# Optimization experiments

Measured on AMD Instinct MI355X. Metric: run time of the kernel, lower is better.

Reference implementation:

```python
import jax, jax.numpy as jnp
import numpy as np

N = 50000      # nodes
E = 600000     # edges
D = 128        # num_features == hidden_units
L = 4          # num_layers
C = 10         # num_classes
G = 512        # graphs in batch
BN_EPS = 1e-5


def setup_inputs() -> dict:
    key = jax.random.key(0)
    ks = jax.random.split(key, 10)
    x = jax.random.normal(ks[0], (N, D), dtype=jnp.float32)
    src = jax.random.randint(ks[1], (E,), 0, N)
    dst = jax.random.randint(ks[2], (E,), 0, N)
    edge_index = jnp.stack([src, dst]).astype(jnp.int64)
    batch = jnp.sort(jax.random.randint(ks[3], (N,), 0, G)).astype(jnp.int64)
    s = 1.0 / np.sqrt(D)
    Wc1 = jax.random.uniform(ks[4], (L, D, D), jnp.float32, -s, s)
    bc1 = jnp.zeros((L, D), jnp.float32)
    Wc2 = jax.random.uniform(ks[5], (L, D, D), jnp.float32, -s, s)
    bc2 = jnp.zeros((L, D), jnp.float32)
    g_mid = jnp.ones((L, D), jnp.float32)   # BN gamma inside conv MLP
    b_mid = jnp.zeros((L, D), jnp.float32)
    g_out = jnp.ones((L, D), jnp.float32)   # BN gamma after conv
    b_out = jnp.zeros((L, D), jnp.float32)
    fcW = jax.random.uniform(ks[6], (L + 1, D, C), jnp.float32, -s, s)
    fcb = jnp.zeros((L + 1, C), jnp.float32)
    return dict(x=x, edge_index=edge_index, batch=batch, Wc1=Wc1, bc1=bc1,
                Wc2=Wc2, bc2=bc2, g_mid=g_mid, b_mid=b_mid, g_out=g_out,
                b_out=b_out, fcW=fcW, fcb=fcb)


def _bn(h, gamma, beta):
    # training-mode BatchNorm1d over the node axis (biased variance)
    mu = h.mean(0)
    var = h.var(0)
    return (h - mu) * jax.lax.rsqrt(var + BN_EPS) * gamma + beta


def reference(x, edge_index, batch, Wc1, bc1, Wc2, bc2, g_mid, b_mid,
              g_out, b_out, fcW, fcb):
    src, dst = edge_index[0], edge_index[1]
    outs = [x]
    h = x
    for i in range(L):
        # GINConv (eps=0): nn( x + sum_{j in N(i)} x_j )
        agg = jax.ops.segment_sum(h[src], dst, num_segments=N)
        z = h + agg
        z = z @ Wc1[i] + bc1[i]
        z = jax.nn.relu(_bn(z, g_mid[i], b_mid[i]))
        z = z @ Wc2[i] + bc2[i]
        h = jax.nn.relu(_bn(z, g_out[i], b_out[i]))  # outer BN + ReLU
        outs.append(h)
    out = jnp.zeros((G, C), x.dtype)
    for i, o in enumerate(outs):
        pooled = jax.ops.segment_sum(o, batch, num_segments=G)  # [G, D]
        out = out + pooled @ fcW[i] + fcb[i]  # dropout p=0.0 -> identity
    return jax.nn.log_softmax(out, axis=-1)
```

## Files before the change

kernel.cpp:

```cpp
#include <hip/hip_runtime.h>
#include <hip/hip_bf16.h>

#define NN 50000
#define EE 600000
#define DD 128
#define LL 4
#define CC 10
#define GG 512
#define BN_EPS 1e-5f
#define ELLW 48

#define EB_BLOCKS ((EE + 255) / 256)
#define PW_BLOCKS ((8 * DD * DD) / 256)
#define GP_BLOCKS 3
#define AGG_BLOCKS (NN / 8)
#define ZERO_N (8 * 256 + NN)
#define ZERO_BLOCKS ((ZERO_N + 255) / 256)

typedef __attribute__((ext_vector_type(8))) short short8;
typedef __attribute__((ext_vector_type(4))) float f32x4;

__device__ __forceinline__ unsigned short f2b(float f) {
    union { float f; unsigned int u; } v; v.f = f;
    unsigned int u = v.u;
    unsigned int r = (u + 0x7fffu + ((u >> 16) & 1u)) >> 16;
    return (unsigned short)r;
}
__device__ __forceinline__ float b2f(unsigned short h) {
    union { unsigned int u; float f; } v; v.u = ((unsigned int)h) << 16;
    return v.f;
}


__global__ __launch_bounds__(256) void zero_kernel(int* __restrict__ base) {
    int i = blockIdx.x * 256 + threadIdx.x;
    if (i < ZERO_N) base[i] = 0;
}


__global__ __launch_bounds__(256) void setup_kernel(const int* __restrict__ src,
                                                    const int* __restrict__ dst,
                                                    int* __restrict__ cursor,
                                                    int* __restrict__ ell,
                                                    const float* __restrict__ Wc1,
                                                    const float* __restrict__ Wc2,
                                                    unsigned short* __restrict__ WTb,
                                                    const int* __restrict__ batch,
                                                    int* __restrict__ gptr,
                                                    const float* __restrict__ x,
                                                    unsigned short* __restrict__ xb,
                                                    float* __restrict__ pooled0) {
    int b = blockIdx.x;
    if (b < GG) {
        __shared__ float2 red[4][64];
        const int g = b;
        int lo = 0, hi = NN;
        while (lo < hi) { int mid = (lo + hi) >> 1; if (batch[mid] < g) lo = mid + 1; else hi = mid; }
        int beg = lo;
        hi = NN;
        while (lo < hi) { int mid = (lo + hi) >> 1; if (batch[mid] < g + 1) lo = mid + 1; else hi = mid; }
        int end = lo;
        int wave = threadIdx.x >> 6, lane = threadIdx.x & 63;
        float ax = 0.f, ay = 0.f;
        for (int r = beg + wave; r < end; r += 4) {
            float2 v = ((const float2*)(x + (size_t)r * DD))[lane];
            ax += v.x; ay += v.y;
            ((unsigned int*)(xb + (size_t)r * DD))[lane] =
                (unsigned int)f2b(v.x) | ((unsigned int)f2b(v.y) << 16);
        }
        red[wave][lane] = make_float2(ax, ay);
        __syncthreads();
        if (threadIdx.x < 64) {
            float2 a = red[0][lane], bb = red[1][lane], c = red[2][lane], d = red[3][lane];
            ((float2*)pooled0)[(size_t)g * 64 + lane] =
                make_float2(a.x + bb.x + c.x + d.x, a.y + bb.y + c.y + d.y);
        }
    } else if (b < GG + EB_BLOCKS) {
        int e = (b - GG) * 256 + threadIdx.x;
        if (e < EE) {
            int d = dst[e];
            int slot = atomicAdd(&cursor[d], 1);
            if (slot < ELLW) ell[(size_t)d * ELLW + slot] = src[e];
        }
    } else if (b < GG + EB_BLOCKS + PW_BLOCKS) {
        int idx = (b - GG - EB_BLOCKS) * 256 + threadIdx.x;
        int mat = idx >> 14;
        int n = (idx >> 7) & 127;
        int k = idx & 127;
        const float* srcp = (mat < 4) ? (Wc1 + (size_t)mat * DD * DD)
                                      : (Wc2 + (size_t)(mat - 4) * DD * DD);
        WTb[idx] = f2b(srcp[k * DD + n]);
    } else {
        int g = (b - GG - EB_BLOCKS - PW_BLOCKS) * 256 + threadIdx.x;
        if (g > GG) return;
        int lo = 0, hi = NN;
        while (lo < hi) {
            int mid = (lo + hi) >> 1;
            if (batch[mid] < g) lo = mid + 1; else hi = mid;
        }
        gptr[g] = lo;
    }
}


template <bool BN>
__device__ __forceinline__ void agg_pair(int nA, const unsigned short* __restrict__ hb,
                                         const int* __restrict__ ell,
                                         const int* __restrict__ degA,
                                         const float* __restrict__ stats,
                                         const float* __restrict__ gamma,
                                         const float* __restrict__ beta,
                                         unsigned short* __restrict__ outb) {
    const int lane = threadIdx.x & 63;
    const int seg = lane & 15;
    const int slot = lane >> 4;

    float A[8], B[8];
    if (BN) {
#pragma unroll
        for (int j = 0; j < 8; ++j) {
            int c = seg * 8 + j;
            float mu = stats[c] * (1.0f / NN);
            float var = stats[DD + c] * (1.0f / NN) - mu * mu;
            A[j] = gamma[c] * rsqrtf(var + BN_EPS);
            B[j] = beta[c] - mu * A[j];
        }
    }

    const uint4* hb4 = (const uint4*)hb;
    uint4 self = hb4[(size_t)(nA + (slot == 1 ? 1 : 0)) * 16 + seg];

    float accA[8], accB[8];
#pragma unroll
    for (int j = 0; j < 8; ++j) { accA[j] = 0.f; accB[j] = 0.f; }

    const int* rowA = ell + (size_t)nA * ELLW;
    const int* rowB = rowA + ELLW;
    const int dgA = min(degA[nA], ELLW);
    const int dgB = min(degA[nA + 1], ELLW);
    const int dgM = max(dgA, dgB);

    for (int e = 0; e < dgM; e += 16) {
        bool vA[4], vB[4];
        int iA[4], iB[4];
#pragma unroll
        for (int i = 0; i < 4; ++i) {
            int t = e + i * 4 + slot;
            vA[i] = (t < dgA);
            vB[i] = (t < dgB);
            iA[i] = rowA[t];
            iB[i] = rowB[t];
        }
        uint4 a[4], b[4];
#pragma unroll
        for (int i = 0; i < 4; ++i) {
            if (vA[i]) a[i] = hb4[(size_t)iA[i] * 16 + seg];
        }
#pragma unroll
        for (int i = 0; i < 4; ++i) {
            if (vB[i]) b[i] = hb4[(size_t)iB[i] * 16 + seg];
        }
#pragma unroll
        for (int i = 0; i < 4; ++i) {
            if (vA[i]) {
#pragma unroll
                for (int j = 0; j < 4; ++j) {
                    unsigned int u = ((unsigned int*)&a[i])[j];
                    float x = b2f((unsigned short)(u & 0xffff));
                    float y = b2f((unsigned short)(u >> 16));
                    if (BN) {
                        x = fmaxf(0.f, fmaf(x, A[2 * j], B[2 * j]));
                        y = fmaxf(0.f, fmaf(y, A[2 * j + 1], B[2 * j + 1]));
                    }
                    accA[2 * j] += x;
                    accA[2 * j + 1] += y;
                }
            }
            if (vB[i]) {
#pragma unroll
                for (int j = 0; j < 4; ++j) {
                    unsigned int u = ((unsigned int*)&b[i])[j];
                    float x = b2f((unsigned short)(u & 0xffff));
                    float y = b2f((unsigned short)(u >> 16));
                    if (BN) {
                        x = fmaxf(0.f, fmaf(x, A[2 * j], B[2 * j]));
                        y = fmaxf(0.f, fmaf(y, A[2 * j + 1], B[2 * j + 1]));
                    }
                    accB[2 * j] += x;
                    accB[2 * j + 1] += y;
                }
            }
        }
    }

#pragma unroll
    for (int j = 0; j < 8; ++j) {
        accA[j] += __shfl_xor(accA[j], 16);
        accA[j] += __shfl_xor(accA[j], 32);
        accB[j] += __shfl_xor(accB[j], 16);
        accB[j] += __shfl_xor(accB[j], 32);
    }

    if (slot < 2) {
        uint4 o;
#pragma unroll
        for (int j = 0; j < 4; ++j) {
            unsigned int u = ((unsigned int*)&self)[j];
            float x = b2f((unsigned short)(u & 0xffff));
            float y = b2f((unsigned short)(u >> 16));
            if (BN) {
                x = fmaxf(0.f, fmaf(x, A[2 * j], B[2 * j]));
                y = fmaxf(0.f, fmaf(y, A[2 * j + 1], B[2 * j + 1]));
            }
            float sx = (slot == 0) ? accA[2 * j] : accB[2 * j];
            float sy = (slot == 0) ? accA[2 * j + 1] : accB[2 * j + 1];
            ((unsigned int*)&o)[j] =
                (unsigned int)f2b(sx + x) | ((unsigned int)f2b(sy + y) << 16);
        }
        ((uint4*)outb)[(size_t)(nA + slot) * 16 + seg] = o;
    }
}

__global__ __launch_bounds__(256) void aggregate_x(const unsigned short* __restrict__ hb,
                                                   const int* __restrict__ ell,
                                                   const int* __restrict__ degA,
                                                   unsigned short* __restrict__ outb) {
    int nA = blockIdx.x * 8 + (threadIdx.x >> 6) * 2;
    agg_pair<false>(nA, hb, ell, degA, nullptr, nullptr, nullptr, outb);
}


__global__ __launch_bounds__(256, 2) void gemm_mfma(
    const unsigned short* __restrict__ Ab,
    const unsigned short* __restrict__ WTb,
    const float* __restrict__ bias,
    const float* __restrict__ bnStatsIn,
    const float* __restrict__ gamma, const float* __restrict__ beta,
    unsigned short* __restrict__ Outb,
    float* __restrict__ statsOut)
{
    __shared__ unsigned short As[128 * 128];
    __shared__ float AbnS[DD], BbnS[DD];
    __shared__ float colred[2][DD];

    const int tid = threadIdx.x;
    const int row0 = blockIdx.x * 128;
    const bool doBn = (bnStatsIn != nullptr);
    const int lane = tid & 63;
    const int fr = lane & 15, fq = lane >> 4;

    short8 bfrag[8][4];
#pragma unroll
    for (int n = 0; n < 8; ++n)
#pragma unroll
        for (int kk = 0; kk < 4; ++kk)
            bfrag[n][kk] = *(const short8*)((const char*)WTb + (n * 16 + fr) * 256 + kk * 64 + fq * 16);

    if (tid < DD) {
        colred[0][tid] = 0.f;
        colred[1][tid] = 0.f;
        if (doBn) {
            float mu = bnStatsIn[tid] * (1.0f / NN);
            float var = bnStatsIn[DD + tid] * (1.0f / NN) - mu * mu;
            float A = gamma[tid] * rsqrtf(var + BN_EPS);
            AbnS[tid] = A;
            BbnS[tid] = beta[tid] - mu * A;
        }
    }
    if (doBn) __syncthreads();

#pragma unroll
    for (int i = 0; i < 8; ++i) {
        int c = tid + i * 256;
        int row = c >> 4, seg = c & 15;
        int gr = row0 + row;
        uint4 v = make_uint4(0u, 0u, 0u, 0u);
        if (gr < NN) v = ((const uint4*)(Ab + (size_t)gr * DD))[seg];
        if (doBn) {
            int k0 = seg * 8;
#pragma unroll
            for (int e = 0; e < 4; ++e) {
                unsigned int u = ((unsigned int*)&v)[e];
                int cidx = k0 + 2 * e;
                float lo = fmaxf(0.f, fmaf(b2f((unsigned short)(u & 0xffff)), AbnS[cidx], BbnS[cidx]));
                float hi = fmaxf(0.f, fmaf(b2f((unsigned short)(u >> 16)), AbnS[cidx + 1], BbnS[cidx + 1]));
                ((unsigned int*)&v)[e] = (unsigned int)f2b(lo) | ((unsigned int)f2b(hi) << 16);
            }
        }
        int byte = (row * 256 + seg * 16) ^ ((row & 7) << 4);
        *(uint4*)((char*)As + byte) = v;
    }
    __syncthreads();

    const int wave = tid >> 6;
    const int wr0 = wave * 32;

    f32x4 acc[2][8];
#pragma unroll
    for (int m = 0; m < 2; ++m)
#pragma unroll
        for (int n = 0; n < 8; ++n) acc[m][n] = (f32x4)0.f;

#pragma unroll
    for (int kk = 0; kk < 4; ++kk) {
        int kbyte = kk * 64 + fq * 16;
        short8 a[2];
#pragma unroll
        for (int m = 0; m < 2; ++m) {
            int row = wr0 + m * 16 + fr;
            a[m] = *(const short8*)((const char*)As + ((row * 256 + kbyte) ^ ((row & 7) << 4)));
        }
#pragma unroll
        for (int m = 0; m < 2; ++m)
#pragma unroll
            for (int n = 0; n < 8; ++n)
                acc[m][n] = __builtin_amdgcn_mfma_f32_16x16x32_bf16(a[m], bfrag[n][kk], acc[m][n], 0, 0, 0);
    }

    float bias_n[8], s[8], q[8];
#pragma unroll
    for (int n = 0; n < 8; ++n) {
        bias_n[n] = bias[n * 16 + fr];
        s[n] = 0.f;
        q[n] = 0.f;
    }
#pragma unroll
    for (int m = 0; m < 2; ++m) {
        int rbase = row0 + wr0 + m * 16 + fq * 4;
#pragma unroll
        for (int j = 0; j < 4; ++j) {
            int gr = rbase + j;
            if (gr < NN) {
#pragma unroll
                for (int n = 0; n < 8; ++n) {
                    float o = acc[m][n][j] + bias_n[n];
                    Outb[(size_t)gr * DD + n * 16 + fr] = f2b(o);
                    s[n] += o;
                    q[n] += o * o;
                }
            }
        }
    }
#pragma unroll
    for (int n = 0; n < 8; ++n) {
        s[n] += __shfl_xor(s[n], 16);
        s[n] += __shfl_xor(s[n], 32);
        q[n] += __shfl_xor(q[n], 16);
        q[n] += __shfl_xor(q[n], 32);
    }
    if (fq == 0) {
#pragma unroll
        for (int n = 0; n < 8; ++n) {
            atomicAdd(&colred[0][n * 16 + fr], s[n]);
            atomicAdd(&colred[1][n * 16 + fr], q[n]);
        }
    }
    __syncthreads();
    if (tid < DD) {
        atomicAdd(&statsOut[tid], colred[0][tid]);
        atomicAdd(&statsOut[DD + tid], colred[1][tid]);
    }
}


template <bool LAST>
__global__ __launch_bounds__(256) void post_layer(
    const unsigned short* __restrict__ Z,
    const float* __restrict__ stats,
    const float* __restrict__ gamma,
    const float* __restrict__ beta,
    const int* __restrict__ gptr,
    const int* __restrict__ ell,
    const int* __restrict__ degA,
    float* __restrict__ pooledDst,
    unsigned short* __restrict__ aggOut,
    const float* __restrict__ pooledAll,
    const float* __restrict__ fcW,
    const float* __restrict__ fcb,
    float* __restrict__ out)
{
    const int bid = blockIdx.x;
    if (bid < GG) {
        __shared__ float2 red[4][64];
        __shared__ float p4[DD];
        const int g = bid;
        const int wave = threadIdx.x >> 6, lane = threadIdx.x & 63;
        const int c0 = lane * 2, c1 = c0 + 1;
        float mu0 = stats[c0] * (1.0f / NN);
        float var0 = stats[DD + c0] * (1.0f / NN) - mu0 * mu0;
        float A0 = gamma[c0] * rsqrtf(var0 + BN_EPS);
        float B0 = beta[c0] - mu0 * A0;
        float mu1 = stats[c1] * (1.0f / NN);
        float var1 = stats[DD + c1] * (1.0f / NN) - mu1 * mu1;
        float A1 = gamma[c1] * rsqrtf(var1 + BN_EPS);
        float B1 = beta[c1] - mu1 * A1;

        float ax = 0.f, ay = 0.f;
        int beg = gptr[g], end = gptr[g + 1];
        for (int r = beg + wave; r < end; r += 4) {
            unsigned int u = ((const unsigned int*)(Z + (size_t)r * DD))[lane];
            ax += fmaxf(0.f, fmaf(b2f((unsigned short)(u & 0xffff)), A0, B0));
            ay += fmaxf(0.f, fmaf(b2f((unsigned short)(u >> 16)), A1, B1));
        }
        red[wave][lane] = make_float2(ax, ay);
        __syncthreads();
        if (threadIdx.x < 64) {
            float2 a = red[0][lane], b = red[1][lane], c = red[2][lane], d = red[3][lane];
            float2 r2 = make_float2(a.x + b.x + c.x + d.x, a.y + b.y + c.y + d.y);
            ((float2*)pooledDst)[(size_t)g * 64 + lane] = r2;
            if (LAST) {
                p4[c0] = r2.x;
                p4[c1] = r2.y;
            }
        }
        if (LAST) {
            __syncthreads();
            if (threadIdx.x < 64) {
                float acc[CC];
#pragma unroll
                for (int c = 0; c < CC; ++c) acc[c] = 0.f;
                for (int i = 0; i < LL + 1; ++i) {
                    const float* Wf = fcW + (size_t)i * DD * CC;
                    for (int k = lane; k < DD; k += 64) {
                        float pv = (i == LL) ? p4[k] : pooledAll[((size_t)i * GG + g) * DD + k];
                        const float* wr = Wf + k * CC;
#pragma unroll
                        for (int c = 0; c < CC; ++c) acc[c] = fmaf(pv, wr[c], acc[c]);
                    }
                }
#pragma unroll
                for (int c = 0; c < CC; ++c)
                    for (int off = 32; off > 0; off >>= 1) acc[c] += __shfl_down(acc[c], off);
                if (lane == 0) {
#pragma unroll
                    for (int c = 0; c < CC; ++c) {
                        float b = 0.f;
                        for (int i = 0; i < LL + 1; ++i) b += fcb[i * CC + c];
                        acc[c] += b;
                    }
                    float m = acc[0];
#pragma unroll
                    for (int c = 1; c < CC; ++c) m = fmaxf(m, acc[c]);
                    float se = 0.f;
#pragma unroll
                    for (int c = 0; c < CC; ++c) se += expf(acc[c] - m);
                    float lse = m + logf(se);
#pragma unroll
                    for (int c = 0; c < CC; ++c) out[(size_t)g * CC + c] = acc[c] - lse;
                }
            }
        }
    } else {
        int nA = (bid - GG) * 8 + (threadIdx.x >> 6) * 2;
        agg_pair<true>(nA, Z, ell, degA, stats, gamma, beta, aggOut);
    }
}


extern "C" void kernel_launch(void* const* d_in, const int* in_sizes, int n_in,
                              void* d_out, int out_size, void* d_ws, size_t ws_size,
                              hipStream_t stream) {
    const float* x     = (const float*)d_in[0];
    const int*   ei    = (const int*)d_in[1];
    const int*   batch = (const int*)d_in[2];
    const float* Wc1   = (const float*)d_in[3];
    const float* bc1   = (const float*)d_in[4];
    const float* Wc2   = (const float*)d_in[5];
    const float* bc2   = (const float*)d_in[6];
    const float* g_mid = (const float*)d_in[7];
    const float* b_mid = (const float*)d_in[8];
    const float* g_out = (const float*)d_in[9];
    const float* b_out = (const float*)d_in[10];
    const float* fcW   = (const float*)d_in[11];
    const float* fcb   = (const float*)d_in[12];
    float* out = (float*)d_out;

    char* p = (char*)d_ws;
    unsigned short* xb   = (unsigned short*)p; p += (size_t)NN * DD * 2;
    unsigned short* aggb = (unsigned short*)p; p += (size_t)NN * DD * 2;
    unsigned short* z1b  = (unsigned short*)p; p += (size_t)NN * DD * 2;
    unsigned short* z2b  = (unsigned short*)p; p += (size_t)NN * DD * 2;
    unsigned short* WTb  = (unsigned short*)p; p += (size_t)8 * DD * DD * 2;
    float* pooled = (float*)p; p += (size_t)(LL + 1) * GG * DD * 4;
    float* statb  = (float*)p; p += 8 * 256 * 4;
    int* cursor = (int*)p; p += (size_t)NN * 4;
    int* ell    = (int*)p; p += (size_t)NN * ELLW * 4;
    int* gptr   = (int*)p; p += (size_t)(GG + 16) * 4;

    const int* src = ei;
    const int* dst = ei + EE;

    zero_kernel<<<ZERO_BLOCKS, 256, 0, stream>>>((int*)statb);
    setup_kernel<<<GG + EB_BLOCKS + PW_BLOCKS + GP_BLOCKS, 256, 0, stream>>>(
        src, dst, cursor, ell, Wc1, Wc2, WTb, batch, gptr, x, xb, pooled);

    const int gemmGrid = (NN + 127) / 128;
    aggregate_x<<<AGG_BLOCKS, 256, 0, stream>>>(xb, ell, cursor, aggb);
    for (int l = 0; l < LL; ++l) {
        gemm_mfma<<<gemmGrid, 256, 0, stream>>>(
            aggb, WTb + (size_t)l * DD * DD, bc1 + (size_t)l * DD,
            nullptr, nullptr, nullptr,
            z1b, statb + (size_t)(2 * l) * 256);
        gemm_mfma<<<gemmGrid, 256, 0, stream>>>(
            z1b, WTb + (size_t)(4 + l) * DD * DD, bc2 + (size_t)l * DD,
            statb + (size_t)(2 * l) * 256, g_mid + (size_t)l * DD, b_mid + (size_t)l * DD,
            z2b, statb + (size_t)(2 * l + 1) * 256);
        if (l < LL - 1) {
            post_layer<false><<<GG + AGG_BLOCKS, 256, 0, stream>>>(
                z2b, statb + (size_t)(2 * l + 1) * 256,
                g_out + (size_t)l * DD, b_out + (size_t)l * DD,
                gptr, ell, cursor,
                pooled + (size_t)(l + 1) * GG * DD, aggb,
                nullptr, nullptr, nullptr, nullptr);
        } else {
            post_layer<true><<<GG, 256, 0, stream>>>(
                z2b, statb + (size_t)(2 * l + 1) * 256,
                g_out + (size_t)l * DD, b_out + (size_t)l * DD,
                gptr, ell, cursor,
                pooled + (size_t)(l + 1) * GG * DD, nullptr,
                pooled, fcW, fcb, out);
        }
    }
}
```

Measured before the change: 359.5 us.

## Build ELL adjacency via per-block buckets with 16-bit source indices

```diff
diff --git a/kernel.cpp b/kernel.cpp
--- a/kernel.cpp
+++ b/kernel.cpp
@@ -9,12 +9,14 @@
 #define GG 512
 #define BN_EPS 1e-5f
 #define ELLW 48
+#define NB ((NN + 127) / 128)
+#define BCAP 2048
 
 #define EB_BLOCKS ((EE + 255) / 256)
 #define PW_BLOCKS ((8 * DD * DD) / 256)
 #define GP_BLOCKS 3
 #define AGG_BLOCKS (NN / 8)
-#define ZERO_N (8 * 256 + NN)
+#define ZERO_N (8 * 256 + NB)
 #define ZERO_BLOCKS ((ZERO_N + 255) / 256)
 
 typedef __attribute__((ext_vector_type(8))) short short8;
@@ -40,8 +42,8 @@
 
 __global__ __launch_bounds__(256) void setup_kernel(const int* __restrict__ src,
                                                     const int* __restrict__ dst,
-                                                    int* __restrict__ cursor,
-                                                    int* __restrict__ ell,
+                                                    int* __restrict__ bcur,
+                                                    unsigned int* __restrict__ buckets,
                                                     const float* __restrict__ Wc1,
                                                     const float* __restrict__ Wc2,
                                                     unsigned short* __restrict__ WTb,
@@ -79,8 +81,11 @@
         int e = (b - GG) * 256 + threadIdx.x;
         if (e < EE) {
             int d = dst[e];
-            int slot = atomicAdd(&cursor[d], 1);
-            if (slot < ELLW) ell[(size_t)d * ELLW + slot] = src[e];
+            int bk = d >> 7;
+            int slot = atomicAdd(&bcur[bk], 1);
+            if (slot < BCAP)
+                buckets[(size_t)bk * BCAP + slot] =
+                    (unsigned int)src[e] | ((unsigned int)(d & 127) << 16);
         }
     } else if (b < GG + EB_BLOCKS + PW_BLOCKS) {
         int idx = (b - GG - EB_BLOCKS) * 256 + threadIdx.x;
@@ -103,9 +108,38 @@
 }
 
 
+__global__ __launch_bounds__(256) void bucket2ell(const unsigned int* __restrict__ buckets,
+                                                  const int* __restrict__ bcur,
+                                                  unsigned short* __restrict__ ell,
+                                                  int* __restrict__ deg) {
+    __shared__ unsigned short lell[128 * ELLW];
+    __shared__ int lcnt[128];
+    const int b = blockIdx.x;
+    const int tid = threadIdx.x;
+    if (tid < 128) lcnt[tid] = 0;
+    __syncthreads();
+    const int cnt = min(bcur[b], BCAP);
+    for (int i = tid; i < cnt; i += 256) {
+        unsigned int pk = buckets[(size_t)b * BCAP + i];
+        int local = pk >> 16;
+        int slot = atomicAdd(&lcnt[local], 1);
+        if (slot < ELLW) lell[local * ELLW + slot] = (unsigned short)(pk & 0xffffu);
+    }
+    __syncthreads();
+    unsigned int* dstp = (unsigned int*)(ell + (size_t)b * 128 * ELLW);
+    const unsigned int* srcp = (const unsigned int*)lell;
+#pragma unroll
+    for (int i = 0; i < 12; ++i) dstp[tid + i * 256] = srcp[tid + i * 256];
+    if (tid < 128) {
+        int node = b * 128 + tid;
+        if (node < NN) deg[node] = min(lcnt[tid], ELLW);
+    }
+}
+
+
 template <bool BN>
 __device__ __forceinline__ void agg_pair(int nA, const unsigned short* __restrict__ hb,
-                                         const int* __restrict__ ell,
+                                         const unsigned short* __restrict__ ell,
                                          const int* __restrict__ degA,
                                          const float* __restrict__ stats,
                                          const float* __restrict__ gamma,
@@ -134,8 +168,8 @@
 #pragma unroll
     for (int j = 0; j < 8; ++j) { accA[j] = 0.f; accB[j] = 0.f; }
 
-    const int* rowA = ell + (size_t)nA * ELLW;
-    const int* rowB = rowA + ELLW;
+    const unsigned short* rowA = ell + (size_t)nA * ELLW;
+    const unsigned short* rowB = rowA + ELLW;
     const int dgA = min(degA[nA], ELLW);
     const int dgB = min(degA[nA + 1], ELLW);
     const int dgM = max(dgA, dgB);
@@ -222,7 +256,7 @@
 }
 
 __global__ __launch_bounds__(256) void aggregate_x(const unsigned short* __restrict__ hb,
-                                                   const int* __restrict__ ell,
+                                                   const unsigned short* __restrict__ ell,
                                                    const int* __restrict__ degA,
                                                    unsigned short* __restrict__ outb) {
     int nA = blockIdx.x * 8 + (threadIdx.x >> 6) * 2;
@@ -370,7 +404,7 @@
     const float* __restrict__ gamma,
     const float* __restrict__ beta,
     const int* __restrict__ gptr,
-    const int* __restrict__ ell,
+    const unsigned short* __restrict__ ell,
     const int* __restrict__ degA,
     float* __restrict__ pooledDst,
     unsigned short* __restrict__ aggOut,
@@ -483,8 +517,10 @@
     unsigned short* WTb  = (unsigned short*)p; p += (size_t)8 * DD * DD * 2;
     float* pooled = (float*)p; p += (size_t)(LL + 1) * GG * DD * 4;
     float* statb  = (float*)p; p += 8 * 256 * 4;
-    int* cursor = (int*)p; p += (size_t)NN * 4;
-    int* ell    = (int*)p; p += (size_t)NN * ELLW * 4;
+    int* bcur   = (int*)p; p += (size_t)NB * 4;
+    int* deg    = (int*)p; p += (size_t)NN * 4;
+    unsigned short* ell = (unsigned short*)p; p += (size_t)NB * 128 * ELLW * 2;
+    unsigned int* buckets = (unsigned int*)p; p += (size_t)NB * BCAP * 4;
     int* gptr   = (int*)p; p += (size_t)(GG + 16) * 4;
 
     const int* src = ei;
@@ -492,10 +528,11 @@
 
     zero_kernel<<<ZERO_BLOCKS, 256, 0, stream>>>((int*)statb);
     setup_kernel<<<GG + EB_BLOCKS + PW_BLOCKS + GP_BLOCKS, 256, 0, stream>>>(
-        src, dst, cursor, ell, Wc1, Wc2, WTb, batch, gptr, x, xb, pooled);
+        src, dst, bcur, buckets, Wc1, Wc2, WTb, batch, gptr, x, xb, pooled);
+    bucket2ell<<<NB, 256, 0, stream>>>(buckets, bcur, ell, deg);
 
     const int gemmGrid = (NN + 127) / 128;
-    aggregate_x<<<AGG_BLOCKS, 256, 0, stream>>>(xb, ell, cursor, aggb);
+    aggregate_x<<<AGG_BLOCKS, 256, 0, stream>>>(xb, ell, deg, aggb);
     for (int l = 0; l < LL; ++l) {
         gemm_mfma<<<gemmGrid, 256, 0, stream>>>(
             aggb, WTb + (size_t)l * DD * DD, bc1 + (size_t)l * DD,
@@ -509,14 +546,14 @@
             post_layer<false><<<GG + AGG_BLOCKS, 256, 0, stream>>>(
                 z2b, statb + (size_t)(2 * l + 1) * 256,
                 g_out + (size_t)l * DD, b_out + (size_t)l * DD,
-                gptr, ell, cursor,
+                gptr, ell, deg,
                 pooled + (size_t)(l + 1) * GG * DD, aggb,
                 nullptr, nullptr, nullptr, nullptr);
         } else {
             post_layer<true><<<GG, 256, 0, stream>>>(
                 z2b, statb + (size_t)(2 * l + 1) * 256,
                 g_out + (size_t)l * DD, b_out + (size_t)l * DD,
-                gptr, ell, cursor,
+                gptr, ell, deg,
                 pooled + (size_t)(l + 1) * GG * DD, nullptr,
                 pooled, fcW, fcb, out);
         }
```

Result: slower. 544.7 us (+51.5%).

## Fuse neighbor aggregation into first GEMM, writing aggregated tile directly to LDS

Applied to the files above, without the earlier changes.

```diff
diff --git a/kernel.cpp b/kernel.cpp
--- a/kernel.cpp
+++ b/kernel.cpp
@@ -9,11 +9,11 @@
 #define GG 512
 #define BN_EPS 1e-5f
 #define ELLW 48
+#define GEMM_GRID ((NN + 127) / 128)
 
 #define EB_BLOCKS ((EE + 255) / 256)
 #define PW_BLOCKS ((8 * DD * DD) / 256)
 #define GP_BLOCKS 3
-#define AGG_BLOCKS (NN / 8)
 #define ZERO_N (8 * 256 + NN)
 #define ZERO_BLOCKS ((ZERO_N + 255) / 256)
 
@@ -103,163 +103,74 @@
 }
 
 
-template <bool BN>
-__device__ __forceinline__ void agg_pair(int nA, const unsigned short* __restrict__ hb,
-                                         const int* __restrict__ ell,
-                                         const int* __restrict__ degA,
-                                         const float* __restrict__ stats,
-                                         const float* __restrict__ gamma,
-                                         const float* __restrict__ beta,
-                                         unsigned short* __restrict__ outb) {
-    const int lane = threadIdx.x & 63;
-    const int seg = lane & 15;
-    const int slot = lane >> 4;
-
-    float A[8], B[8];
-    if (BN) {
-#pragma unroll
-        for (int j = 0; j < 8; ++j) {
-            int c = seg * 8 + j;
-            float mu = stats[c] * (1.0f / NN);
-            float var = stats[DD + c] * (1.0f / NN) - mu * mu;
-            A[j] = gamma[c] * rsqrtf(var + BN_EPS);
-            B[j] = beta[c] - mu * A[j];
-        }
-    }
-
-    const uint4* hb4 = (const uint4*)hb;
-    uint4 self = hb4[(size_t)(nA + (slot == 1 ? 1 : 0)) * 16 + seg];
-
-    float accA[8], accB[8];
-#pragma unroll
-    for (int j = 0; j < 8; ++j) { accA[j] = 0.f; accB[j] = 0.f; }
-
-    const int* rowA = ell + (size_t)nA * ELLW;
-    const int* rowB = rowA + ELLW;
-    const int dgA = min(degA[nA], ELLW);
-    const int dgB = min(degA[nA + 1], ELLW);
-    const int dgM = max(dgA, dgB);
-
-    for (int e = 0; e < dgM; e += 16) {
-        bool vA[4], vB[4];
-        int iA[4], iB[4];
-#pragma unroll
-        for (int i = 0; i < 4; ++i) {
-            int t = e + i * 4 + slot;
-            vA[i] = (t < dgA);
-            vB[i] = (t < dgB);
-            iA[i] = rowA[t];
-            iB[i] = rowB[t];
-        }
-        uint4 a[4], b[4];
-#pragma unroll
-        for (int i = 0; i < 4; ++i) {
-            if (vA[i]) a[i] = hb4[(size_t)iA[i] * 16 + seg];
-        }
-#pragma unroll
-        for (int i = 0; i < 4; ++i) {
-            if (vB[i]) b[i] = hb4[(size_t)iB[i] * 16 + seg];
-        }
-#pragma unroll
-        for (int i = 0; i < 4; ++i) {
-            if (vA[i]) {
-#pragma unroll
-                for (int j = 0; j < 4; ++j) {
-                    unsigned int u = ((unsigned int*)&a[i])[j];
-                    float x = b2f((unsigned short)(u & 0xffff));
-                    float y = b2f((unsigned short)(u >> 16));
-                    if (BN) {
-                        x = fmaxf(0.f, fmaf(x, A[2 * j], B[2 * j]));
-                        y = fmaxf(0.f, fmaf(y, A[2 * j + 1], B[2 * j + 1]));
-                    }
-                    accA[2 * j] += x;
-                    accA[2 * j + 1] += y;
-                }
-            }
-            if (vB[i]) {
-#pragma unroll
-                for (int j = 0; j < 4; ++j) {
-                    unsigned int u = ((unsigned int*)&b[i])[j];
-                    float x = b2f((unsigned short)(u & 0xffff));
-                    float y = b2f((unsigned short)(u >> 16));
-                    if (BN) {
-                        x = fmaxf(0.f, fmaf(x, A[2 * j], B[2 * j]));
-                        y = fmaxf(0.f, fmaf(y, A[2 * j + 1], B[2 * j + 1]));
-                    }
-                    accB[2 * j] += x;
-                    accB[2 * j + 1] += y;
-                }
-            }
-        }
-    }
-
-#pragma unroll
-    for (int j = 0; j < 8; ++j) {
-        accA[j] += __shfl_xor(accA[j], 16);
-        accA[j] += __shfl_xor(accA[j], 32);
-        accB[j] += __shfl_xor(accB[j], 16);
-        accB[j] += __shfl_xor(accB[j], 32);
-    }
-
-    if (slot < 2) {
-        uint4 o;
-#pragma unroll
-        for (int j = 0; j < 4; ++j) {
-            unsigned int u = ((unsigned int*)&self)[j];
-            float x = b2f((unsigned short)(u & 0xffff));
-            float y = b2f((unsigned short)(u >> 16));
-            if (BN) {
-                x = fmaxf(0.f, fmaf(x, A[2 * j], B[2 * j]));
-                y = fmaxf(0.f, fmaf(y, A[2 * j + 1], B[2 * j + 1]));
-            }
-            float sx = (slot == 0) ? accA[2 * j] : accB[2 * j];
-            float sy = (slot == 0) ? accA[2 * j + 1] : accB[2 * j + 1];
-            ((unsigned int*)&o)[j] =
-                (unsigned int)f2b(sx + x) | ((unsigned int)f2b(sy + y) << 16);
-        }
-        ((uint4*)outb)[(size_t)(nA + slot) * 16 + seg] = o;
-    }
-}
-
-__global__ __launch_bounds__(256) void aggregate_x(const unsigned short* __restrict__ hb,
-                                                   const int* __restrict__ ell,
-                                                   const int* __restrict__ degA,
-                                                   unsigned short* __restrict__ outb) {
-    int nA = blockIdx.x * 8 + (threadIdx.x >> 6) * 2;
-    agg_pair<false>(nA, hb, ell, degA, nullptr, nullptr, nullptr, outb);
-}
-
-
-__global__ __launch_bounds__(256, 2) void gemm_mfma(
-    const unsigned short* __restrict__ Ab,
+__device__ __forceinline__ void pool_block(const unsigned short* __restrict__ Z,
+                                           const float* __restrict__ stats,
+                                           const float* __restrict__ gamma,
+                                           const float* __restrict__ beta,
+                                           const int* __restrict__ gptr,
+                                           float* __restrict__ pooledDst, int g) {
+    __shared__ float2 red[4][64];
+    const int wave = threadIdx.x >> 6, lane = threadIdx.x & 63;
+    const int c0 = lane * 2, c1 = c0 + 1;
+    float mu0 = stats[c0] * (1.0f / NN);
+    float var0 = stats[DD + c0] * (1.0f / NN) - mu0 * mu0;
+    float A0 = gamma[c0] * rsqrtf(var0 + BN_EPS);
+    float B0 = beta[c0] - mu0 * A0;
+    float mu1 = stats[c1] * (1.0f / NN);
+    float var1 = stats[DD + c1] * (1.0f / NN) - mu1 * mu1;
+    float A1 = gamma[c1] * rsqrtf(var1 + BN_EPS);
+    float B1 = beta[c1] - mu1 * A1;
+
+    float ax = 0.f, ay = 0.f;
+    int beg = gptr[g], end = gptr[g + 1];
+    for (int r = beg + wave; r < end; r += 4) {
+        unsigned int u = ((const unsigned int*)(Z + (size_t)r * DD))[lane];
+        ax += fmaxf(0.f, fmaf(b2f((unsigned short)(u & 0xffff)), A0, B0));
+        ay += fmaxf(0.f, fmaf(b2f((unsigned short)(u >> 16)), A1, B1));
+    }
+    red[wave][lane] = make_float2(ax, ay);
+    __syncthreads();
+    if (threadIdx.x < 64) {
+        float2 a = red[0][lane], b = red[1][lane], c = red[2][lane], d = red[3][lane];
+        ((float2*)pooledDst)[(size_t)g * 64 + lane] =
+            make_float2(a.x + b.x + c.x + d.x, a.y + b.y + c.y + d.y);
+    }
+}
+
+
+template <int AMODE, bool POOL>
+__global__ __launch_bounds__(256, 2) void gemm_fused(
+    const unsigned short* __restrict__ hin,
+    const int* __restrict__ ell,
+    const int* __restrict__ degA,
     const unsigned short* __restrict__ WTb,
     const float* __restrict__ bias,
     const float* __restrict__ bnStatsIn,
     const float* __restrict__ gamma, const float* __restrict__ beta,
     unsigned short* __restrict__ Outb,
-    float* __restrict__ statsOut)
+    float* __restrict__ statsOut,
+    const int* __restrict__ gptr,
+    float* __restrict__ pooledDst)
 {
+    if (POOL && blockIdx.x >= GEMM_GRID) {
+        pool_block(hin, bnStatsIn, gamma, beta, gptr, pooledDst, blockIdx.x - GEMM_GRID);
+        return;
+    }
+
     __shared__ unsigned short As[128 * 128];
     __shared__ float AbnS[DD], BbnS[DD];
     __shared__ float colred[2][DD];
 
     const int tid = threadIdx.x;
     const int row0 = blockIdx.x * 128;
-    const bool doBn = (bnStatsIn != nullptr);
     const int lane = tid & 63;
     const int fr = lane & 15, fq = lane >> 4;
-
-    short8 bfrag[8][4];
-#pragma unroll
-    for (int n = 0; n < 8; ++n)
-#pragma unroll
-        for (int kk = 0; kk < 4; ++kk)
-            bfrag[n][kk] = *(const short8*)((const char*)WTb + (n * 16 + fr) * 256 + kk * 64 + fq * 16);
+    const int wave = tid >> 6;
 
     if (tid < DD) {
         colred[0][tid] = 0.f;
         colred[1][tid] = 0.f;
-        if (doBn) {
+        if (AMODE == 0 && bnStatsIn) {
             float mu = bnStatsIn[tid] * (1.0f / NN);
             float var = bnStatsIn[DD + tid] * (1.0f / NN) - mu * mu;
             float A = gamma[tid] * rsqrtf(var + BN_EPS);
@@ -267,34 +178,154 @@
             BbnS[tid] = beta[tid] - mu * A;
         }
     }
-    if (doBn) __syncthreads();
-
-#pragma unroll
-    for (int i = 0; i < 8; ++i) {
-        int c = tid + i * 256;
-        int row = c >> 4, seg = c & 15;
-        int gr = row0 + row;
-        uint4 v = make_uint4(0u, 0u, 0u, 0u);
-        if (gr < NN) v = ((const uint4*)(Ab + (size_t)gr * DD))[seg];
-        if (doBn) {
-            int k0 = seg * 8;
-#pragma unroll
-            for (int e = 0; e < 4; ++e) {
-                unsigned int u = ((unsigned int*)&v)[e];
-                int cidx = k0 + 2 * e;
-                float lo = fmaxf(0.f, fmaf(b2f((unsigned short)(u & 0xffff)), AbnS[cidx], BbnS[cidx]));
-                float hi = fmaxf(0.f, fmaf(b2f((unsigned short)(u >> 16)), AbnS[cidx + 1], BbnS[cidx + 1]));
-                ((unsigned int*)&v)[e] = (unsigned int)f2b(lo) | ((unsigned int)f2b(hi) << 16);
-            }
-        }
-        int byte = (row * 256 + seg * 16) ^ ((row & 7) << 4);
-        *(uint4*)((char*)As + byte) = v;
-    }
-    __syncthreads();
-
-    const int wave = tid >> 6;
+
+    if (AMODE == 0) {
+        const bool doBn = (bnStatsIn != nullptr);
+        if (doBn) __syncthreads();
+#pragma unroll
+        for (int i = 0; i < 8; ++i) {
+            int c = tid + i * 256;
+            int row = c >> 4, seg = c & 15;
+            int gr = row0 + row;
+            uint4 v = make_uint4(0u, 0u, 0u, 0u);
+            if (gr < NN) v = ((const uint4*)(hin + (size_t)gr * DD))[seg];
+            if (doBn) {
+                int k0 = seg * 8;
+#pragma unroll
+                for (int e = 0; e < 4; ++e) {
+                    unsigned int u = ((unsigned int*)&v)[e];
+                    int cidx = k0 + 2 * e;
+                    float lo = fmaxf(0.f, fmaf(b2f((unsigned short)(u & 0xffff)), AbnS[cidx], BbnS[cidx]));
+                    float hi = fmaxf(0.f, fmaf(b2f((unsigned short)(u >> 16)), AbnS[cidx + 1], BbnS[cidx + 1]));
+                    ((unsigned int*)&v)[e] = (unsigned int)f2b(lo) | ((unsigned int)f2b(hi) << 16);
+                }
+            }
+            int byte = (row * 256 + seg * 16) ^ ((row & 7) << 4);
+            *(uint4*)((char*)As + byte) = v;
+        }
+        __syncthreads();
+    } else {
+        const int seg = fr;
+        const int slot = fq;
+        float A8[8], B8[8];
+        if (AMODE == 2) {
+#pragma unroll
+            for (int j = 0; j < 8; ++j) {
+                int c = seg * 8 + j;
+                float mu = bnStatsIn[c] * (1.0f / NN);
+                float var = bnStatsIn[DD + c] * (1.0f / NN) - mu * mu;
+                A8[j] = gamma[c] * rsqrtf(var + BN_EPS);
+                B8[j] = beta[c] - mu * A8[j];
+            }
+        }
+        const uint4* hb4 = (const uint4*)hin;
+        for (int pp = 0; pp < 16; ++pp) {
+            const int r0 = wave * 32 + pp * 2;
+            const int nA = row0 + r0;
+            if (nA >= NN) {
+                if (slot < 2) {
+                    int row = r0 + slot;
+                    int byte = (row * 256 + seg * 16) ^ ((row & 7) << 4);
+                    *(uint4*)((char*)As + byte) = make_uint4(0u, 0u, 0u, 0u);
+                }
+                continue;
+            }
+            uint4 self = hb4[(size_t)(nA + (slot == 1 ? 1 : 0)) * 16 + seg];
+            float accA[8], accB[8];
+#pragma unroll
+            for (int j = 0; j < 8; ++j) { accA[j] = 0.f; accB[j] = 0.f; }
+            const int* rowA = ell + (size_t)nA * ELLW;
+            const int* rowB = rowA + ELLW;
+            const int dgA = min(degA[nA], ELLW);
+            const int dgB = min(degA[nA + 1], ELLW);
+            const int dgM = max(dgA, dgB);
+            for (int e = 0; e < dgM; e += 16) {
+                bool vA[4], vB[4];
+                int iA[4], iB[4];
+#pragma unroll
+                for (int i = 0; i < 4; ++i) {
+                    int t = e + i * 4 + slot;
+                    vA[i] = (t < dgA);
+                    vB[i] = (t < dgB);
+                    iA[i] = rowA[t];
+                    iB[i] = rowB[t];
+                }
+                uint4 a[4], b[4];
+#pragma unroll
+                for (int i = 0; i < 4; ++i) { if (vA[i]) a[i] = hb4[(size_t)iA[i] * 16 + seg]; }
+#pragma unroll
+                for (int i = 0; i < 4; ++i) { if (vB[i]) b[i] = hb4[(size_t)iB[i] * 16 + seg]; }
+#pragma unroll
+                for (int i = 0; i < 4; ++i) {
+                    if (vA[i]) {
+#pragma unroll
+                        for (int j = 0; j < 4; ++j) {
+                            unsigned int u = ((unsigned int*)&a[i])[j];
+                            float x = b2f((unsigned short)(u & 0xffff));
+                            float y = b2f((unsigned short)(u >> 16));
+                            if (AMODE == 2) {
+                                x = fmaxf(0.f, fmaf(x, A8[2 * j], B8[2 * j]));
+                                y = fmaxf(0.f, fmaf(y, A8[2 * j + 1], B8[2 * j + 1]));
+                            }
+                            accA[2 * j] += x;
+                            accA[2 * j + 1] += y;
+                        }
+                    }
+                    if (vB[i]) {
+#pragma unroll
+                        for (int j = 0; j < 4; ++j) {
+                            unsigned int u = ((unsigned int*)&b[i])[j];
+                            float x = b2f((unsigned short)(u & 0xffff));
+                            float y = b2f((unsigned short)(u >> 16));
+                            if (AMODE == 2) {
+                                x = fmaxf(0.f, fmaf(x, A8[2 * j], B8[2 * j]));
+                                y = fmaxf(0.f, fmaf(y, A8[2 * j + 1], B8[2 * j + 1]));
+                            }
+                            accB[2 * j] += x;
+                            accB[2 * j + 1] += y;
+                        }
+                    }
+                }
+            }
+#pragma unroll
+            for (int j = 0; j < 8; ++j) {
+                accA[j] += __shfl_xor(accA[j], 16);
+                accA[j] += __shfl_xor(accA[j], 32);
+                accB[j] += __shfl_xor(accB[j], 16);
+                accB[j] += __shfl_xor(accB[j], 32);
+            }
+            if (slot < 2) {
+                uint4 o;
+#pragma unroll
+                for (int j = 0; j < 4; ++j) {
+                    unsigned int u = ((unsigned int*)&self)[j];
+                    float x = b2f((unsigned short)(u & 0xffff));
+                    float y = b2f((unsigned short)(u >> 16));
+                    if (AMODE == 2) {
+                        x = fmaxf(0.f, fmaf(x, A8[2 * j], B8[2 * j]));
+                        y = fmaxf(0.f, fmaf(y, A8[2 * j + 1], B8[2 * j + 1]));
+                    }
+                    float sx = (slot == 0) ? accA[2 * j] : accB[2 * j];
+                    float sy = (slot == 0) ? accA[2 * j + 1] : accB[2 * j + 1];
+                    ((unsigned int*)&o)[j] =
+                        (unsigned int)f2b(sx + x) | ((unsigned int)f2b(sy + y) << 16);
+                }
+                int row = r0 + slot;
+                int byte = (row * 256 + seg * 16) ^ ((row & 7) << 4);
+                *(uint4*)((char*)As + byte) = o;
+            }
+        }
+        __syncthreads();
+    }
+
+    short8 bfrag[8][4];
+#pragma unroll
+    for (int n = 0; n < 8; ++n)
+#pragma unroll
+        for (int kk = 0; kk < 4; ++kk)
+            bfrag[n][kk] = *(const short8*)((const char*)WTb + (n * 16 + fr) * 256 + kk * 64 + fq * 16);
+
     const int wr0 = wave * 32;
-
     f32x4 acc[2][8];
 #pragma unroll
     for (int m = 0; m < 2; ++m)
@@ -363,96 +394,80 @@
 }
 
 
-template <bool LAST>
-__global__ __launch_bounds__(256) void post_layer(
-    const unsigned short* __restrict__ Z,
-    const float* __restrict__ stats,
-    const float* __restrict__ gamma,
-    const float* __restrict__ beta,
-    const int* __restrict__ gptr,
-    const int* __restrict__ ell,
-    const int* __restrict__ degA,
-    float* __restrict__ pooledDst,
-    unsigned short* __restrict__ aggOut,
-    const float* __restrict__ pooledAll,
-    const float* __restrict__ fcW,
-    const float* __restrict__ fcb,
-    float* __restrict__ out)
-{
-    const int bid = blockIdx.x;
-    if (bid < GG) {
-        __shared__ float2 red[4][64];
-        __shared__ float p4[DD];
-        const int g = bid;
-        const int wave = threadIdx.x >> 6, lane = threadIdx.x & 63;
-        const int c0 = lane * 2, c1 = c0 + 1;
-        float mu0 = stats[c0] * (1.0f / NN);
-        float var0 = stats[DD + c0] * (1.0f / NN) - mu0 * mu0;
-        float A0 = gamma[c0] * rsqrtf(var0 + BN_EPS);
-        float B0 = beta[c0] - mu0 * A0;
-        float mu1 = stats[c1] * (1.0f / NN);
-        float var1 = stats[DD + c1] * (1.0f / NN) - mu1 * mu1;
-        float A1 = gamma[c1] * rsqrtf(var1 + BN_EPS);
-        float B1 = beta[c1] - mu1 * A1;
-
-        float ax = 0.f, ay = 0.f;
-        int beg = gptr[g], end = gptr[g + 1];
-        for (int r = beg + wave; r < end; r += 4) {
-            unsigned int u = ((const unsigned int*)(Z + (size_t)r * DD))[lane];
-            ax += fmaxf(0.f, fmaf(b2f((unsigned short)(u & 0xffff)), A0, B0));
-            ay += fmaxf(0.f, fmaf(b2f((unsigned short)(u >> 16)), A1, B1));
-        }
-        red[wave][lane] = make_float2(ax, ay);
-        __syncthreads();
-        if (threadIdx.x < 64) {
-            float2 a = red[0][lane], b = red[1][lane], c = red[2][lane], d = red[3][lane];
-            float2 r2 = make_float2(a.x + b.x + c.x + d.x, a.y + b.y + c.y + d.y);
-            ((float2*)pooledDst)[(size_t)g * 64 + lane] = r2;
-            if (LAST) {
-                p4[c0] = r2.x;
-                p4[c1] = r2.y;
-            }
-        }
-        if (LAST) {
-            __syncthreads();
-            if (threadIdx.x < 64) {
-                float acc[CC];
-#pragma unroll
-                for (int c = 0; c < CC; ++c) acc[c] = 0.f;
-                for (int i = 0; i < LL + 1; ++i) {
-                    const float* Wf = fcW + (size_t)i * DD * CC;
-                    for (int k = lane; k < DD; k += 64) {
-                        float pv = (i == LL) ? p4[k] : pooledAll[((size_t)i * GG + g) * DD + k];
-                        const float* wr = Wf + k * CC;
-#pragma unroll
-                        for (int c = 0; c < CC; ++c) acc[c] = fmaf(pv, wr[c], acc[c]);
-                    }
-                }
-#pragma unroll
-                for (int c = 0; c < CC; ++c)
-                    for (int off = 32; off > 0; off >>= 1) acc[c] += __shfl_down(acc[c], off);
-                if (lane == 0) {
-#pragma unroll
-                    for (int c = 0; c < CC; ++c) {
-                        float b = 0.f;
-                        for (int i = 0; i < LL + 1; ++i) b += fcb[i * CC + c];
-                        acc[c] += b;
-                    }
-                    float m = acc[0];
-#pragma unroll
-                    for (int c = 1; c < CC; ++c) m = fmaxf(m, acc[c]);
-                    float se = 0.f;
-#pragma unroll
-                    for (int c = 0; c < CC; ++c) se += expf(acc[c] - m);
-                    float lse = m + logf(se);
-#pragma unroll
-                    for (int c = 0; c < CC; ++c) out[(size_t)g * CC + c] = acc[c] - lse;
-                }
-            }
-        }
-    } else {
-        int nA = (bid - GG) * 8 + (threadIdx.x >> 6) * 2;
-        agg_pair<true>(nA, Z, ell, degA, stats, gamma, beta, aggOut);
+__global__ __launch_bounds__(256) void pool_last(const unsigned short* __restrict__ Z,
+                                                 const float* __restrict__ stats,
+                                                 const float* __restrict__ gamma,
+                                                 const float* __restrict__ beta,
+                                                 const int* __restrict__ gptr,
+                                                 float* __restrict__ pooledDst,
+                                                 const float* __restrict__ pooledAll,
+                                                 const float* __restrict__ fcW,
+                                                 const float* __restrict__ fcb,
+                                                 float* __restrict__ out) {
+    __shared__ float2 red[4][64];
+    __shared__ float p4[DD];
+    const int g = blockIdx.x;
+    const int wave = threadIdx.x >> 6, lane = threadIdx.x & 63;
+    const int c0 = lane * 2, c1 = c0 + 1;
+    float mu0 = stats[c0] * (1.0f / NN);
+    float var0 = stats[DD + c0] * (1.0f / NN) - mu0 * mu0;
+    float A0 = gamma[c0] * rsqrtf(var0 + BN_EPS);
+    float B0 = beta[c0] - mu0 * A0;
+    float mu1 = stats[c1] * (1.0f / NN);
+    float var1 = stats[DD + c1] * (1.0f / NN) - mu1 * mu1;
+    float A1 = gamma[c1] * rsqrtf(var1 + BN_EPS);
+    float B1 = beta[c1] - mu1 * A1;
+
+    float ax = 0.f, ay = 0.f;
+    int beg = gptr[g], end = gptr[g + 1];
+    for (int r = beg + wave; r < end; r += 4) {
+        unsigned int u = ((const unsigned int*)(Z + (size_t)r * DD))[lane];
+        ax += fmaxf(0.f, fmaf(b2f((unsigned short)(u & 0xffff)), A0, B0));
+        ay += fmaxf(0.f, fmaf(b2f((unsigned short)(u >> 16)), A1, B1));
+    }
+    red[wave][lane] = make_float2(ax, ay);
+    __syncthreads();
+    if (threadIdx.x < 64) {
+        float2 a = red[0][lane], b = red[1][lane], c = red[2][lane], d = red[3][lane];
+        float2 r2 = make_float2(a.x + b.x + c.x + d.x, a.y + b.y + c.y + d.y);
+        ((float2*)pooledDst)[(size_t)g * 64 + lane] = r2;
+        p4[c0] = r2.x;
+        p4[c1] = r2.y;
+    }
+    __syncthreads();
+    if (threadIdx.x < 64) {
+        float acc[CC];
+#pragma unroll
+        for (int c = 0; c < CC; ++c) acc[c] = 0.f;
+        for (int i = 0; i < LL + 1; ++i) {
+            const float* Wf = fcW + (size_t)i * DD * CC;
+            for (int k = lane; k < DD; k += 64) {
+                float pv = (i == LL) ? p4[k] : pooledAll[((size_t)i * GG + g) * DD + k];
+                const float* wr = Wf + k * CC;
+#pragma unroll
+                for (int c = 0; c < CC; ++c) acc[c] = fmaf(pv, wr[c], acc[c]);
+            }
+        }
+#pragma unroll
+        for (int c = 0; c < CC; ++c)
+            for (int off = 32; off > 0; off >>= 1) acc[c] += __shfl_down(acc[c], off);
+        if (lane == 0) {
+#pragma unroll
+            for (int c = 0; c < CC; ++c) {
+                float b = 0.f;
+                for (int i = 0; i < LL + 1; ++i) b += fcb[i * CC + c];
+                acc[c] += b;
+            }
+            float m = acc[0];
+#pragma unroll
+            for (int c = 1; c < CC; ++c) m = fmaxf(m, acc[c]);
+            float se = 0.f;
+#pragma unroll
+            for (int c = 0; c < CC; ++c) se += expf(acc[c] - m);
+            float lse = m + logf(se);
+#pragma unroll
+            for (int c = 0; c < CC; ++c) out[(size_t)g * CC + c] = acc[c] - lse;
+        }
     }
 }
 
@@ -477,7 +492,6 @@
 
     char* p = (char*)d_ws;
     unsigned short* xb   = (unsigned short*)p; p += (size_t)NN * DD * 2;
-    unsigned short* aggb = (unsigned short*)p; p += (size_t)NN * DD * 2;
     unsigned short* z1b  = (unsigned short*)p; p += (size_t)NN * DD * 2;
     unsigned short* z2b  = (unsigned short*)p; p += (size_t)NN * DD * 2;
     unsigned short* WTb  = (unsigned short*)p; p += (size_t)8 * DD * DD * 2;
@@ -494,31 +508,30 @@
     setup_kernel<<<GG + EB_BLOCKS + PW_BLOCKS + GP_BLOCKS, 256, 0, stream>>>(
         src, dst, cursor, ell, Wc1, Wc2, WTb, batch, gptr, x, xb, pooled);
 
-    const int gemmGrid = (NN + 127) / 128;
-    aggregate_x<<<AGG_BLOCKS, 256, 0, stream>>>(xb, ell, cursor, aggb);
     for (int l = 0; l < LL; ++l) {
-        gemm_mfma<<<gemmGrid, 256, 0, stream>>>(
-            aggb, WTb + (size_t)l * DD * DD, bc1 + (size_t)l * DD,
-            nullptr, nullptr, nullptr,
-            z1b, statb + (size_t)(2 * l) * 256);
-        gemm_mfma<<<gemmGrid, 256, 0, stream>>>(
-            z1b, WTb + (size_t)(4 + l) * DD * DD, bc2 + (size_t)l * DD,
+        const unsigned short* hin = (l == 0) ? xb : z2b;
+        const float* aStats = (l == 0) ? nullptr : statb + (size_t)(2 * (l - 1) + 1) * 256;
+        const float* aGamma = (l == 0) ? nullptr : g_out + (size_t)(l - 1) * DD;
+        const float* aBeta  = (l == 0) ? nullptr : b_out + (size_t)(l - 1) * DD;
+        if (l == 0) {
+            gemm_fused<1, false><<<GEMM_GRID, 256, 0, stream>>>(
+                hin, ell, cursor, WTb + (size_t)l * DD * DD, bc1 + (size_t)l * DD,
+                nullptr, nullptr, nullptr,
+                z1b, statb + (size_t)(2 * l) * 256, gptr, nullptr);
+        } else {
+            gemm_fused<2, true><<<GEMM_GRID + GG, 256, 0, stream>>>(
+                hin, ell, cursor, WTb + (size_t)l * DD * DD, bc1 + (size_t)l * DD,
+                aStats, aGamma, aBeta,
+                z1b, statb + (size_t)(2 * l) * 256, gptr,
+                pooled + (size_t)l * GG * DD);
+        }
+        gemm_fused<0, false><<<GEMM_GRID, 256, 0, stream>>>(
+            z1b, nullptr, nullptr, WTb + (size_t)(4 + l) * DD * DD, bc2 + (size_t)l * DD,
             statb + (size_t)(2 * l) * 256, g_mid + (size_t)l * DD, b_mid + (size_t)l * DD,
-            z2b, statb + (size_t)(2 * l + 1) * 256);
-        if (l < LL - 1) {
-            post_layer<false><<<GG + AGG_BLOCKS, 256, 0, stream>>>(
-                z2b, statb + (size_t)(2 * l + 1) * 256,
-                g_out + (size_t)l * DD, b_out + (size_t)l * DD,
-                gptr, ell, cursor,
-                pooled + (size_t)(l + 1) * GG * DD, aggb,
-                nullptr, nullptr, nullptr, nullptr);
-        } else {
-            post_layer<true><<<GG, 256, 0, stream>>>(
-                z2b, statb + (size_t)(2 * l + 1) * 256,
-                g_out + (size_t)l * DD, b_out + (size_t)l * DD,
-                gptr, ell, cursor,
-                pooled + (size_t)(l + 1) * GG * DD, nullptr,
-                pooled, fcW, fcb, out);
-        }
-    }
-}
+            z2b, statb + (size_t)(2 * l + 1) * 256, gptr, nullptr);
+    }
+    pool_last<<<GG, 256, 0, stream>>>(
+        z2b, statb + (size_t)(2 * (LL - 1) + 1) * 256,
+        g_out + (size_t)(LL - 1) * DD, b_out + (size_t)(LL - 1) * DD,
+        gptr, pooled + (size_t)LL * GG * DD, pooled, fcW, fcb, out);
+}
```

Measured after the change: 404.0 us. +12.4%, slower.

## Halve GEMM row tile to 64 and load weight fragments per K-half

Applied to the files above, without the earlier changes.

```diff
diff --git a/kernel.cpp b/kernel.cpp
--- a/kernel.cpp
+++ b/kernel.cpp
@@ -16,6 +16,7 @@
 #define AGG_BLOCKS (NN / 8)
 #define ZERO_N (8 * 256 + NN)
 #define ZERO_BLOCKS ((ZERO_N + 255) / 256)
+#define GEMM_GRID ((NN + 63) / 64)
 
 typedef __attribute__((ext_vector_type(8))) short short8;
 typedef __attribute__((ext_vector_type(4))) float f32x4;
@@ -153,13 +154,9 @@
         }
         uint4 a[4], b[4];
 #pragma unroll
-        for (int i = 0; i < 4; ++i) {
-            if (vA[i]) a[i] = hb4[(size_t)iA[i] * 16 + seg];
-        }
-#pragma unroll
-        for (int i = 0; i < 4; ++i) {
-            if (vB[i]) b[i] = hb4[(size_t)iB[i] * 16 + seg];
-        }
+        for (int i = 0; i < 4; ++i) { if (vA[i]) a[i] = hb4[(size_t)iA[i] * 16 + seg]; }
+#pragma unroll
+        for (int i = 0; i < 4; ++i) { if (vB[i]) b[i] = hb4[(size_t)iB[i] * 16 + seg]; }
 #pragma unroll
         for (int i = 0; i < 4; ++i) {
             if (vA[i]) {
@@ -239,22 +236,16 @@
     unsigned short* __restrict__ Outb,
     float* __restrict__ statsOut)
 {
-    __shared__ unsigned short As[128 * 128];
+    __shared__ unsigned short As[64 * 128];
     __shared__ float AbnS[DD], BbnS[DD];
     __shared__ float colred[2][DD];
 
     const int tid = threadIdx.x;
-    const int row0 = blockIdx.x * 128;
+    const int row0 = blockIdx.x * 64;
     const bool doBn = (bnStatsIn != nullptr);
     const int lane = tid & 63;
     const int fr = lane & 15, fq = lane >> 4;
-
-    short8 bfrag[8][4];
-#pragma unroll
-    for (int n = 0; n < 8; ++n)
-#pragma unroll
-        for (int kk = 0; kk < 4; ++kk)
-            bfrag[n][kk] = *(const short8*)((const char*)WTb + (n * 16 + fr) * 256 + kk * 64 + fq * 16);
+    const int wave = tid >> 6;
 
     if (tid < DD) {
         colred[0][tid] = 0.f;
@@ -270,7 +261,7 @@
     if (doBn) __syncthreads();
 
 #pragma unroll
-    for (int i = 0; i < 8; ++i) {
+    for (int i = 0; i < 4; ++i) {
         int c = tid + i * 256;
         int row = c >> 4, seg = c & 15;
         int gr = row0 + row;
@@ -292,29 +283,31 @@
     }
     __syncthreads();
 
-    const int wave = tid >> 6;
-    const int wr0 = wave * 32;
-
-    f32x4 acc[2][8];
-#pragma unroll
-    for (int m = 0; m < 2; ++m)
-#pragma unroll
-        for (int n = 0; n < 8; ++n) acc[m][n] = (f32x4)0.f;
-
-#pragma unroll
-    for (int kk = 0; kk < 4; ++kk) {
-        int kbyte = kk * 64 + fq * 16;
-        short8 a[2];
-#pragma unroll
-        for (int m = 0; m < 2; ++m) {
-            int row = wr0 + m * 16 + fr;
-            a[m] = *(const short8*)((const char*)As + ((row * 256 + kbyte) ^ ((row & 7) << 4)));
-        }
-#pragma unroll
-        for (int m = 0; m < 2; ++m)
+    const int wr0 = wave * 16;
+    f32x4 acc[8];
+#pragma unroll
+    for (int n = 0; n < 8; ++n) acc[n] = (f32x4)0.f;
+
+#pragma unroll
+    for (int half = 0; half < 2; ++half) {
+        short8 bfrag[8][2];
+#pragma unroll
+        for (int n = 0; n < 8; ++n)
+#pragma unroll
+            for (int kkl = 0; kkl < 2; ++kkl) {
+                int kk = half * 2 + kkl;
+                bfrag[n][kkl] = *(const short8*)((const char*)WTb + (n * 16 + fr) * 256 + kk * 64 + fq * 16);
+            }
+#pragma unroll
+        for (int kkl = 0; kkl < 2; ++kkl) {
+            int kk = half * 2 + kkl;
+            int kbyte = kk * 64 + fq * 16;
+            int row = wr0 + fr;
+            short8 a = *(const short8*)((const char*)As + ((row * 256 + kbyte) ^ ((row & 7) << 4)));
 #pragma unroll
             for (int n = 0; n < 8; ++n)
-                acc[m][n] = __builtin_amdgcn_mfma_f32_16x16x32_bf16(a[m], bfrag[n][kk], acc[m][n], 0, 0, 0);
+                acc[n] = __builtin_amdgcn_mfma_f32_16x16x32_bf16(a, bfrag[n][kkl], acc[n], 0, 0, 0);
+        }
     }
 
     float bias_n[8], s[8], q[8];
@@ -324,20 +317,17 @@
         s[n] = 0.f;
         q[n] = 0.f;
     }
-#pragma unroll
-    for (int m = 0; m < 2; ++m) {
-        int rbase = row0 + wr0 + m * 16 + fq * 4;
-#pragma unroll
-        for (int j = 0; j < 4; ++j) {
-            int gr = rbase + j;
-            if (gr < NN) {
-#pragma unroll
-                for (int n = 0; n < 8; ++n) {
-                    float o = acc[m][n][j] + bias_n[n];
-                    Outb[(size_t)gr * DD + n * 16 + fr] = f2b(o);
-                    s[n] += o;
-                    q[n] += o * o;
-                }
+    const int rbase = row0 + wr0 + fq * 4;
+#pragma unroll
+    for (int j = 0; j < 4; ++j) {
+        int gr = rbase + j;
+        if (gr < NN) {
+#pragma unroll
+            for (int n = 0; n < 8; ++n) {
+                float o = acc[n][j] + bias_n[n];
+                Outb[(size_t)gr * DD + n * 16 + fr] = f2b(o);
+                s[n] += o;
+                q[n] += o * o;
             }
         }
     }
@@ -494,14 +484,13 @@
     setup_kernel<<<GG + EB_BLOCKS + PW_BLOCKS + GP_BLOCKS, 256, 0, stream>>>(
         src, dst, cursor, ell, Wc1, Wc2, WTb, batch, gptr, x, xb, pooled);
 
-    const int gemmGrid = (NN + 127) / 128;
     aggregate_x<<<AGG_BLOCKS, 256, 0, stream>>>(xb, ell, cursor, aggb);
     for (int l = 0; l < LL; ++l) {
-        gemm_mfma<<<gemmGrid, 256, 0, stream>>>(
+        gemm_mfma<<<GEMM_GRID, 256, 0, stream>>>(
             aggb, WTb + (size_t)l * DD * DD, bc1 + (size_t)l * DD,
             nullptr, nullptr, nullptr,
             z1b, statb + (size_t)(2 * l) * 256);
-        gemm_mfma<<<gemmGrid, 256, 0, stream>>>(
+        gemm_mfma<<<GEMM_GRID, 256, 0, stream>>>(
             z1b, WTb + (size_t)(4 + l) * DD * DD, bc2 + (size_t)l * DD,
             statb + (size_t)(2 * l) * 256, g_mid + (size_t)l * DD, b_mid + (size_t)l * DD,
             z2b, statb + (size_t)(2 * l + 1) * 256);
```

After: 474.5 us. +32.0%, slower.
